# Kernel optimization log

Measured on AMD Instinct MI355X. Metric: run time of the kernel, lower is better.

The kernel has to match this reference:

```python
import jax, jax.numpy as jnp
import numpy as np

B, N, D, C = 1, 512, 128, 128
EPS = 1e-5


def _layernorm(x, g, b):
    m = jnp.mean(x, axis=-1, keepdims=True)
    v = jnp.mean(jnp.square(x - m), axis=-1, keepdims=True)
    return (x - m) * jax.lax.rsqrt(v + EPS) * g + b


def setup_inputs() -> dict:
    key = jax.random.key(0)
    ks = jax.random.split(key, 14)
    sD = 1.0 / np.sqrt(D)
    sC = 1.0 / np.sqrt(C)

    def w(k, shape, scale):
        return jax.random.normal(k, shape, dtype=jnp.float32) * scale

    return {
        "x": jax.random.normal(ks[0], (B, N, N, D), dtype=jnp.float32),
        "ln_in_g": jnp.ones((D,), jnp.float32),
        "ln_in_b": jnp.zeros((D,), jnp.float32),
        "ln_out_g": jnp.ones((C,), jnp.float32),
        "ln_out_b": jnp.zeros((C,), jnp.float32),
        "Wl": w(ks[1], (D, C), sD), "bl": w(ks[2], (C,), 0.02),
        "Wr": w(ks[3], (D, C), sD), "br": w(ks[4], (C,), 0.02),
        "Wo": w(ks[5], (C, D), sC), "bo": w(ks[6], (D,), 0.02),
        "Wlg": w(ks[7], (D, C), sD), "blg": w(ks[8], (C,), 0.02),
        "Wrg": w(ks[9], (D, C), sD), "brg": w(ks[10], (C,), 0.02),
        "Wog": w(ks[11], (D, D), sD), "bog": w(ks[12], (D,), 0.02),
    }


def reference(x, ln_in_g, ln_in_b, ln_out_g, ln_out_b,
              Wl, bl, Wr, br, Wo, bo, Wlg, blg, Wrg, brg, Wog, bog):
    # x: [B, N, N, D] pair representation
    xn = _layernorm(x, ln_in_g, ln_in_b)
    left = jax.nn.sigmoid(xn @ Wlg + blg) * (xn @ Wl + bl)    # [B,N,N,C]
    right = jax.nn.sigmoid(xn @ Wrg + brg) * (xn @ Wr + br)   # [B,N,N,C]
    # type='out': contract over k (rows): out[b,i,j,c] = sum_k left[b,k,i,c]*right[b,k,j,c]
    out = jnp.einsum('bkic,bkjc->bijc', left, right)           # [B,N,N,C]
    out = jax.nn.sigmoid(xn @ Wog + bog) * (_layernorm(out, ln_out_g, ln_out_b) @ Wo + bo)
    return out
```

## Files before the change

kernel.cpp:

```cpp
#include <hip/hip_runtime.h>
#include <hip/hip_bf16.h>
#include <cstdint>
#include <cstddef>

typedef unsigned short u16;
typedef short bf16x8 __attribute__((ext_vector_type(8)));
typedef float f32x4 __attribute__((ext_vector_type(4)));

constexpr int Ns = 512;
constexpr int Dd = 128;
constexpr int Cc = 128;
#define EPSV 1e-5f

__device__ __forceinline__ u16 f2bf(float f){
    __hip_bfloat16 h = __float2bfloat16(f);
    return *reinterpret_cast<u16*>(&h);
}
__device__ __forceinline__ float bf2f(u16 h){
    return __uint_as_float(((uint32_t)h) << 16);
}
__device__ __forceinline__ float sigmoidf_(float x){
    return __builtin_amdgcn_rcpf(1.0f + __expf(-x));
}

#define LDS_FENCE do {                                         \
    asm volatile("s_waitcnt lgkmcnt(0)" ::: "memory");         \
    __builtin_amdgcn_sched_barrier(0);                         \
} while (0)

__global__ void k_prep(const float* __restrict__ Wl, const float* __restrict__ Wlg,
                       const float* __restrict__ Wr, const float* __restrict__ Wrg,
                       const float* __restrict__ Wog, const float* __restrict__ Wo,
                       u16* __restrict__ Wt){
    int idx = blockIdx.x * 256 + threadIdx.x;
    if (idx >= 6 * 16384) return;
    int m = idx >> 14; int nk = idx & 16383; int n = nk >> 7; int k = nk & 127;
    const float* W = (m == 0) ? Wl : (m == 1) ? Wlg : (m == 2) ? Wr
                   : (m == 3) ? Wrg : (m == 4) ? Wog : Wo;
    Wt[idx] = f2bf(W[k * Cc + n]);
}

__global__ __launch_bounds__(256) void k1(
    const float* __restrict__ x, const float* __restrict__ g_ln, const float* __restrict__ b_ln,
    const u16* __restrict__ Wt,
    const float* __restrict__ bl, const float* __restrict__ blg,
    const float* __restrict__ br, const float* __restrict__ brg,
    const float* __restrict__ bog,
    u16* __restrict__ left, u16* __restrict__ right, u16* __restrict__ og)
{
    __shared__ u16  SB[8704];
    __shared__ float gln[128], bln[128];

    const int t   = threadIdx.x;
    const int bid = blockIdx.x;
    const int a0  = (bid >> 6) << 3;
    const int b0  = (bid & 63) << 3;
    const int w = t >> 6, l = t & 63;
    const int lrow = l & 15, g = l >> 4;
    const int nb = w * 32;
    const int orow = g << 2;
    const int kb = a0 >> 3;

    const int r = t >> 2, q = t & 3;
    const int aa = a0 + (r & 7), bb = b0 + (r >> 3);
    const float4* xrow = reinterpret_cast<const float4*>(x + ((size_t)aa * Ns + bb) * Dd);
    float4 xv[8];
#pragma unroll
    for (int i2 = 0; i2 < 8; ++i2) xv[i2] = xrow[q + 4 * i2];
    if (t < 128){ gln[t] = g_ln[t]; bln[t] = b_ln[t]; }

    float s1 = 0.f, s2 = 0.f;
#pragma unroll
    for (int i2 = 0; i2 < 8; ++i2){
        float4 v = xv[i2];
        s1 += v.x + v.y + v.z + v.w;
        s2 += v.x * v.x + v.y * v.y + v.z * v.z + v.w * v.w;
    }
    s1 += __shfl_xor(s1, 1); s1 += __shfl_xor(s1, 2);
    s2 += __shfl_xor(s2, 1); s2 += __shfl_xor(s2, 2);
    const float mm  = s1 * (1.0f / 128.0f);
    const float rsv = rsqrtf(s2 * (1.0f / 128.0f) - mm * mm + EPSV);
    __syncthreads();
#pragma unroll
    for (int i2 = 0; i2 < 8; ++i2){
        const int d = (q + 4 * i2) * 4;
        ushort4 o;
        o.x = f2bf((xv[i2].x - mm) * rsv * gln[d + 0] + bln[d + 0]);
        o.y = f2bf((xv[i2].y - mm) * rsv * gln[d + 1] + bln[d + 1]);
        o.z = f2bf((xv[i2].z - mm) * rsv * gln[d + 2] + bln[d + 2]);
        o.w = f2bf((xv[i2].w - mm) * rsv * gln[d + 3] + bln[d + 3]);
        *reinterpret_cast<ushort4*>(&SB[r * 136 + d]) = o;
    }
    __syncthreads();

    bf16x8 af[4][4];
#pragma unroll
    for (int ks = 0; ks < 4; ++ks)
#pragma unroll
        for (int rf = 0; rf < 4; ++rf)
            af[ks][rf] = *reinterpret_cast<const bf16x8*>(&SB[(rf * 16 + lrow) * 136 + ks * 32 + g * 8]);
    __syncthreads();

    u16* SBw = &SB[w * 32 * 68];
    const f32x4 zero4 = {0.f, 0.f, 0.f, 0.f};
    f32x4 aV[4], aG[4];

    auto GEMM1 = [&](const u16* WV, const u16* WG, int cf){
        const int col = nb + cf * 16 + lrow;
#pragma unroll
        for (int rf = 0; rf < 4; ++rf){ aV[rf] = zero4; aG[rf] = zero4; }
#pragma unroll
        for (int ks = 0; ks < 4; ++ks){
            bf16x8 bv = *reinterpret_cast<const bf16x8*>(WV + (size_t)col * 128 + ks * 32 + g * 8);
            bf16x8 bg = *reinterpret_cast<const bf16x8*>(WG + (size_t)col * 128 + ks * 32 + g * 8);
#pragma unroll
            for (int rf = 0; rf < 4; ++rf)
                aV[rf] = __builtin_amdgcn_mfma_f32_16x16x32_bf16(af[ks][rf], bv, aV[rf], 0, 0, 0);
#pragma unroll
            for (int rf = 0; rf < 4; ++rf)
                aG[rf] = __builtin_amdgcn_mfma_f32_16x16x32_bf16(af[ks][rf], bg, aG[rf], 0, 0, 0);
        }
    };
    auto STW = [&](const float* bV, const float* bG, int cf){
        const int cl2 = cf * 16 + lrow;
        const int col = nb + cl2;
        const float bVv = bV[col], bGv = bG[col];
#pragma unroll
        for (int rf = 0; rf < 4; ++rf){
            ushort4 pk;
#pragma unroll
            for (int j = 0; j < 4; ++j){
                const float vv = aV[rf][j] + bVv;
                const float gg = aG[rf][j] + bGv;
                ((u16*)&pk)[j] = f2bf(sigmoidf_(gg) * vv);
            }
            *reinterpret_cast<ushort4*>(&SBw[cl2 * 68 + rf * 16 + orow]) = pk;
        }
    };
    auto STORE = [&](u16* dst){
#pragma unroll
        for (int it = 0; it < 4; ++it){
            const int cl2 = it * 8 + (l >> 3);
            const int s   = l & 7;
            int4 v = *reinterpret_cast<const int4*>(&SBw[cl2 * 68 + s * 8]);
            *reinterpret_cast<int4*>(dst + (((size_t)(nb + cl2) * 64 + kb) * Ns + b0) * 8 + s * 8) = v;
        }
    };

    GEMM1(Wt,             Wt + 16384,     0); STW(bl, blg, 0);
    GEMM1(Wt,             Wt + 16384,     1); STW(bl, blg, 1);
    LDS_FENCE;
    STORE(left);
    LDS_FENCE;
    GEMM1(Wt + 2 * 16384, Wt + 3 * 16384, 0); STW(br, brg, 0);
    GEMM1(Wt + 2 * 16384, Wt + 3 * 16384, 1); STW(br, brg, 1);
    LDS_FENCE;
    STORE(right);
    __syncthreads();

    const u16* WO = Wt + (size_t)4 * 16384;
#pragma unroll 1
    for (int cf = 0; cf < 2; ++cf){
        const int col = nb + cf * 16 + lrow;
#pragma unroll
        for (int rf = 0; rf < 4; ++rf) aV[rf] = zero4;
#pragma unroll
        for (int ks = 0; ks < 4; ++ks){
            bf16x8 bv = *reinterpret_cast<const bf16x8*>(WO + (size_t)col * 128 + ks * 32 + g * 8);
#pragma unroll
            for (int rf = 0; rf < 4; ++rf)
                aV[rf] = __builtin_amdgcn_mfma_f32_16x16x32_bf16(af[ks][rf], bv, aV[rf], 0, 0, 0);
        }
        const float bOv = bog[col];
#pragma unroll
        for (int rf = 0; rf < 4; ++rf)
#pragma unroll
            for (int j = 0; j < 4; ++j){
                const int row = rf * 16 + orow + j;
                SB[row * 132 + col] = f2bf(sigmoidf_(aV[rf][j] + bOv));
            }
    }
    __syncthreads();
    const int bsub = t >> 5, c4 = (t & 31) * 4;
#pragma unroll
    for (int a = 0; a < 8; ++a){
        const int row = bsub * 8 + a;
        int2 v = *reinterpret_cast<const int2*>(&SB[row * 132 + c4]);
        *reinterpret_cast<int2*>(og + (((size_t)(a0 + a) * Ns) + (b0 + bsub)) * Cc + c4) = v;
    }
}

#define K2_LOAD(AF, BF, KS) do {                                                    \
    const size_t kbrow_ = (size_t)((KS) * 4 + lkb) * Ns;                            \
    _Pragma("unroll") for (int rf = 0; rf < 4; ++rf)                                \
        AF[rf] = *reinterpret_cast<const bf16x8*>(Lc + (kbrow_ + ib + rf * 16 + lrow) * 8); \
    _Pragma("unroll") for (int cf = 0; cf < 4; ++cf)                                \
        BF[cf] = *reinterpret_cast<const bf16x8*>(Rc + (kbrow_ + jb + cf * 16 + lrow) * 8); \
} while (0)

#define K2_MM(AF, BF) do {                                                          \
    _Pragma("unroll") for (int rf = 0; rf < 4; ++rf)                                \
    _Pragma("unroll") for (int cf = 0; cf < 4; ++cf)                                \
        acc[rf][cf] = __builtin_amdgcn_mfma_f32_16x16x32_bf16(AF[rf], BF[cf], acc[rf][cf], 0, 0, 0); \
} while (0)

__global__ __launch_bounds__(256) void k2(const u16* __restrict__ left,
                                          const u16* __restrict__ right,
                                          u16* __restrict__ om)
{
    __shared__ u16 sO[128][136];
    const int bid = blockIdx.x;
    const int xcd = bid & 7, idxx = bid >> 3;
    const int virt = xcd * 256 + idxx;
    const int c    = virt >> 4;
    const int tile = virt & 15;
    const int iy = tile >> 2, jx = tile & 3;
    const int t = threadIdx.x, w = t >> 6, l = t & 63;
    const int wr = w >> 1, wc = w & 1;
    const int ib = iy * 128 + wr * 64;
    const int jb = jx * 128 + wc * 64;
    const int lrow = l & 15, lkb = l >> 4;
    const u16* Lc = left  + (size_t)c * (Ns * Ns);
    const u16* Rc = right + (size_t)c * (Ns * Ns);
    const f32x4 zero4 = {0.f, 0.f, 0.f, 0.f};
    f32x4 acc[4][4];
#pragma unroll
    for (int rf = 0; rf < 4; ++rf)
#pragma unroll
        for (int cf = 0; cf < 4; ++cf) acc[rf][cf] = zero4;

    bf16x8 a0f[4], b0f[4], a1f[4], b1f[4];
    K2_LOAD(a0f, b0f, 0);
#pragma unroll
    for (int ks = 0; ks < 16; ks += 2){
        K2_LOAD(a1f, b1f, ks + 1);
        K2_MM(a0f, b0f);
        if (ks + 2 < 16) K2_LOAD(a0f, b0f, ks + 2);
        K2_MM(a1f, b1f);
    }

    const int orow = (l >> 4) << 2;
#pragma unroll
    for (int rf = 0; rf < 4; ++rf)
#pragma unroll
        for (int j2 = 0; j2 < 4; ++j2){
            const int rloc = wr * 64 + rf * 16 + orow + j2;
#pragma unroll
            for (int cf = 0; cf < 4; ++cf)
                sO[rloc][wc * 64 + cf * 16 + lrow] = f2bf(acc[rf][cf][j2]);
        }
    __syncthreads();
    u16* obase = om + (size_t)c * Ns * Ns + (size_t)(iy * 128) * Ns + jx * 128;
#pragma unroll
    for (int s = 0; s < 8; ++s){
        const int gg = s * 256 + t;
        const int row = gg >> 4, co = (gg & 15) * 8;
        int4 v = *reinterpret_cast<const int4*>(&sO[row][co]);
        *reinterpret_cast<int4*>(obase + (size_t)row * Ns + co) = v;
    }
}

__global__ __launch_bounds__(256) void k3(
    const u16* __restrict__ om, const u16* __restrict__ og, const u16* __restrict__ Wt,
    const float* __restrict__ g2, const float* __restrict__ b2, const float* __restrict__ bo,
    float* __restrict__ out)
{
    __shared__ char smem[34816];
    u16* X = reinterpret_cast<u16*>(smem);
    u16* O = reinterpret_cast<u16*>(smem) + 8704;
    __shared__ float sg2[128], sb2[128];
    const int i  = blockIdx.y;
    const int j0 = blockIdx.x * 64;
    const int t  = threadIdx.x;
    if (t < 128){ sg2[t] = g2[t]; sb2[t] = b2[t]; }
    {
        const int c = t >> 1, jh = (t & 1) * 32;
        const u16* src = om + (size_t)c * Ns * Ns + (size_t)i * Ns + j0 + jh;
#pragma unroll
        for (int s = 0; s < 8; ++s){
            ushort4 v = reinterpret_cast<const ushort4*>(src)[s];
            const int jj = jh + s * 4;
            X[(jj + 0) * 136 + c] = v.x; X[(jj + 1) * 136 + c] = v.y;
            X[(jj + 2) * 136 + c] = v.z; X[(jj + 3) * 136 + c] = v.w;
        }
    }
    {
        const int jj = t >> 2, qq = t & 3;
        const u16* src = og + ((size_t)i * Ns + j0 + jj) * Cc + qq * 32;
#pragma unroll
        for (int s = 0; s < 4; ++s)
            *reinterpret_cast<int4*>(&O[jj * 136 + qq * 32 + s * 8]) = reinterpret_cast<const int4*>(src)[s];
    }
    __syncthreads();
    const int r = t >> 2, q = t & 3;
    {
        float s1 = 0.f, s2v = 0.f;
#pragma unroll
        for (int e = 0; e < 32; ++e){
            const float v = bf2f(X[r * 136 + q * 32 + e]);
            s1 += v; s2v += v * v;
        }
        s1  += __shfl_xor(s1, 1);  s1  += __shfl_xor(s1, 2);
        s2v += __shfl_xor(s2v, 1); s2v += __shfl_xor(s2v, 2);
        const float mm  = s1 * (1.0f / 128.0f);
        const float rsv = rsqrtf(s2v * (1.0f / 128.0f) - mm * mm + EPSV);
#pragma unroll
        for (int e = 0; e < 32; ++e){
            const int cc = q * 32 + e;
            const float v = bf2f(X[r * 136 + cc]);
            X[r * 136 + cc] = f2bf((v - mm) * rsv * sg2[cc] + sb2[cc]);
        }
    }
    __syncthreads();
    const int w = t >> 6, l = t & 63;
    const int lrow = l & 15, lk = (l >> 4) << 3, nbv = w * 32, orow = (l >> 4) << 2;
    const u16* WO = Wt + (size_t)5 * 16384;
    const f32x4 zero4 = {0.f, 0.f, 0.f, 0.f};
    f32x4 acc[4][2];
#pragma unroll
    for (int rf = 0; rf < 4; ++rf)
#pragma unroll
        for (int cf = 0; cf < 2; ++cf) acc[rf][cf] = zero4;
#pragma unroll
    for (int ks = 0; ks < 4; ++ks){
        const int k0 = ks * 32 + lk;
        bf16x8 af[4];
#pragma unroll
        for (int rf = 0; rf < 4; ++rf)
            af[rf] = *reinterpret_cast<const bf16x8*>(&X[(rf * 16 + lrow) * 136 + k0]);
#pragma unroll
        for (int cf = 0; cf < 2; ++cf){
            bf16x8 bv = *reinterpret_cast<const bf16x8*>(WO + (size_t)(nbv + cf * 16 + lrow) * 128 + k0);
#pragma unroll
            for (int rf = 0; rf < 4; ++rf)
                acc[rf][cf] = __builtin_amdgcn_mfma_f32_16x16x32_bf16(af[rf], bv, acc[rf][cf], 0, 0, 0);
        }
    }
    float gv[2][4][4];
#pragma unroll
    for (int cf = 0; cf < 2; ++cf){
        const int cg = nbv + cf * 16 + lrow;
        const float bov = bo[cg];
#pragma unroll
        for (int rf = 0; rf < 4; ++rf)
#pragma unroll
            for (int j = 0; j < 4; ++j){
                const int row = rf * 16 + orow + j;
                gv[cf][rf][j] = bf2f(O[row * 136 + cg]) * (acc[rf][cf][j] + bov);
            }
    }
    __syncthreads();
    float* sF = reinterpret_cast<float*>(smem);
#pragma unroll
    for (int cf = 0; cf < 2; ++cf){
        const int cg = nbv + cf * 16 + lrow;
#pragma unroll
        for (int rf = 0; rf < 4; ++rf)
#pragma unroll
            for (int j = 0; j < 4; ++j){
                const int row = rf * 16 + orow + j;
                sF[row * 128 + cg] = gv[cf][rf][j];
            }
    }
    __syncthreads();
    const float4* sF4 = reinterpret_cast<const float4*>(smem);
    float* obase = out + ((size_t)i * Ns + j0) * Cc;
#pragma unroll
    for (int s = 0; s < 8; ++s){
        const int gg = s * 256 + t;
        const int row = gg >> 5, co = (gg & 31) * 4;
        float4 v = sF4[gg];
        *reinterpret_cast<float4*>(obase + (size_t)row * Cc + co) = v;
    }
}

extern "C" void kernel_launch(void* const* d_in, const int* in_sizes, int n_in,
                              void* d_out, int out_size, void* d_ws, size_t ws_size,
                              hipStream_t stream)
{
    const float* x    = (const float*)d_in[0];
    const float* ling = (const float*)d_in[1];
    const float* linb = (const float*)d_in[2];
    const float* loutg= (const float*)d_in[3];
    const float* loutb= (const float*)d_in[4];
    const float* Wl   = (const float*)d_in[5];
    const float* bl   = (const float*)d_in[6];
    const float* Wr   = (const float*)d_in[7];
    const float* br   = (const float*)d_in[8];
    const float* Wo   = (const float*)d_in[9];
    const float* bo   = (const float*)d_in[10];
    const float* Wlg  = (const float*)d_in[11];
    const float* blg  = (const float*)d_in[12];
    const float* Wrg  = (const float*)d_in[13];
    const float* brg  = (const float*)d_in[14];
    const float* Wog  = (const float*)d_in[15];
    const float* bog  = (const float*)d_in[16];

    char* ws = (char*)d_ws;
    u16* Wt = (u16*)ws;
    const size_t off = 256 * 1024;
    const size_t SZ  = (size_t)33554432 * 2;
    u16* left  = (u16*)(ws + off);
    u16* right = (u16*)(ws + off + SZ);
    u16* og    = (u16*)(ws + off + 2 * SZ);
    u16* om    = (u16*)(ws + off + 3 * SZ);

    hipLaunchKernelGGL(k_prep, dim3(384), dim3(256), 0, stream, Wl, Wlg, Wr, Wrg, Wog, Wo, Wt);
    hipLaunchKernelGGL(k1, dim3(4096), dim3(256), 0, stream,
                       x, ling, linb, Wt, bl, blg, br, brg, bog, left, right, og);
    hipLaunchKernelGGL(k2, dim3(2048), dim3(256), 0, stream, left, right, om);
    hipLaunchKernelGGL(k3, dim3(8, 512), dim3(256), 0, stream, om, og, Wt, loutg, loutb, bo, (float*)d_out);
}
```

Measured before the change: 254.1 us.

## Double k1 tile to 16x8 pair rows with 512-thread blocks

The k1 block grows from 256 to 512 threads and now handles 16 a-rows by 8 b-columns, with two half-groups of four waves sharing the same weight columns. This halves the grid, so each block fetches the weight fragments once for twice as many rows. The left/right and og store paths are re-indexed so each block writes two kb blocks per column and uses wider int4 stores. In exchange, LDS per block doubles and each write to left/right is split into two shorter contiguous segments, which could hurt coalescing and occupancy.

```diff
diff --git a/kernel.cpp b/kernel.cpp
--- a/kernel.cpp
+++ b/kernel.cpp
@@ -40,7 +40,7 @@
     Wt[idx] = f2bf(W[k * Cc + n]);
 }
 
-__global__ __launch_bounds__(256) void k1(
+__global__ __launch_bounds__(512) void k1(
     const float* __restrict__ x, const float* __restrict__ g_ln, const float* __restrict__ b_ln,
     const u16* __restrict__ Wt,
     const float* __restrict__ bl, const float* __restrict__ blg,
@@ -48,21 +48,22 @@
     const float* __restrict__ bog,
     u16* __restrict__ left, u16* __restrict__ right, u16* __restrict__ og)
 {
-    __shared__ u16  SB[8704];
+    __shared__ u16  SB[17408];
     __shared__ float gln[128], bln[128];
 
     const int t   = threadIdx.x;
     const int bid = blockIdx.x;
-    const int a0  = (bid >> 6) << 3;
+    const int a0  = (bid >> 6) << 4;
     const int b0  = (bid & 63) << 3;
     const int w = t >> 6, l = t & 63;
     const int lrow = l & 15, g = l >> 4;
-    const int nb = w * 32;
+    const int h  = w >> 2;
+    const int nb = (w & 3) * 32;
     const int orow = g << 2;
-    const int kb = a0 >> 3;
+    const int kb2 = a0 >> 3;
 
     const int r = t >> 2, q = t & 3;
-    const int aa = a0 + (r & 7), bb = b0 + (r >> 3);
+    const int aa = a0 + (r & 15), bb = b0 + (r >> 4);
     const float4* xrow = reinterpret_cast<const float4*>(x + ((size_t)aa * Ns + bb) * Dd);
     float4 xv[8];
 #pragma unroll
@@ -98,7 +99,8 @@
     for (int ks = 0; ks < 4; ++ks)
 #pragma unroll
         for (int rf = 0; rf < 4; ++rf)
-            af[ks][rf] = *reinterpret_cast<const bf16x8*>(&SB[(rf * 16 + lrow) * 136 + ks * 32 + g * 8]);
+            af[ks][rf] = *reinterpret_cast<const bf16x8*>(
+                &SB[(h * 64 + rf * 16 + lrow) * 136 + ks * 32 + g * 8]);
     __syncthreads();
 
     u16* SBw = &SB[w * 32 * 68];
@@ -140,10 +142,14 @@
     auto STORE = [&](u16* dst){
 #pragma unroll
         for (int it = 0; it < 4; ++it){
-            const int cl2 = it * 8 + (l >> 3);
-            const int s   = l & 7;
-            int4 v = *reinterpret_cast<const int4*>(&SBw[cl2 * 68 + s * 8]);
-            *reinterpret_cast<int4*>(dst + (((size_t)(nb + cl2) * 64 + kb) * Ns + b0) * 8 + s * 8) = v;
+            const int idx   = it * 64 + l;
+            const int col_l = idx >> 3;
+            const int kbi   = (idx >> 2) & 1;
+            const int b_rel = idx & 3;
+            int4 v = *reinterpret_cast<const int4*>(&SBw[col_l * 68 + b_rel * 16 + kbi * 8]);
+            const size_t base = (((size_t)(nb + col_l) * 64 + kb2 + kbi) * Ns
+                                 + b0 + h * 4 + b_rel) * 8;
+            *reinterpret_cast<int4*>(dst + base) = v;
         }
     };
 
@@ -176,17 +182,19 @@
         for (int rf = 0; rf < 4; ++rf)
 #pragma unroll
             for (int j = 0; j < 4; ++j){
-                const int row = rf * 16 + orow + j;
-                SB[row * 132 + col] = f2bf(sigmoidf_(aV[rf][j] + bOv));
+                const int lr = h * 64 + rf * 16 + orow + j;
+                SB[lr * 132 + col] = f2bf(sigmoidf_(aV[rf][j] + bOv));
             }
     }
     __syncthreads();
-    const int bsub = t >> 5, c4 = (t & 31) * 4;
-#pragma unroll
-    for (int a = 0; a < 8; ++a){
-        const int row = bsub * 8 + a;
-        int2 v = *reinterpret_cast<const int2*>(&SB[row * 132 + c4]);
-        *reinterpret_cast<int2*>(og + (((size_t)(a0 + a) * Ns) + (b0 + bsub)) * Cc + c4) = v;
+    {
+        const int lr = t >> 2, c4 = (t & 3) * 32;
+        const size_t gb = ((size_t)(a0 + (lr & 15)) * Ns + b0 + (lr >> 4)) * Cc + c4;
+#pragma unroll
+        for (int s = 0; s < 4; ++s){
+            int4 v = *reinterpret_cast<const int4*>(&SB[lr * 132 + c4 + s * 8]);
+            *reinterpret_cast<int4*>(og + gb + s * 8) = v;
+        }
     }
 }
 
@@ -406,7 +414,7 @@
     u16* om    = (u16*)(ws + off + 3 * SZ);
 
     hipLaunchKernelGGL(k_prep, dim3(384), dim3(256), 0, stream, Wl, Wlg, Wr, Wrg, Wog, Wo, Wt);
-    hipLaunchKernelGGL(k1, dim3(4096), dim3(256), 0, stream,
+    hipLaunchKernelGGL(k1, dim3(2048), dim3(512), 0, stream,
                        x, ling, linb, Wt, bl, blg, br, brg, bog, left, right, og);
     hipLaunchKernelGGL(k2, dim3(2048), dim3(256), 0, stream, left, right, om);
     hipLaunchKernelGGL(k3, dim3(8, 512), dim3(256), 0, stream, om, og, Wt, loutg, loutb, bo, (float*)d_out);
```

Result: slower. 288.2 us (+13.4%).

## Recompute output gate in final kernel instead of storing gate tensor

Applied to the files above, without the earlier changes.

The output-gate GEMM (xn @ Wog) and its sigmoid move out of the first kernel. The final kernel now rereads x, recomputes the input layernorm, and runs the gate GEMM next to the Wo projection. This removes the bf16 gate intermediate (64 MB written and read back) and the extra shared-memory transpose in k1. In exchange k3 reads fp32 x (128 MB), does the layernorm and GEMM a second time, and uses more registers for the doubled accumulators.

```diff
diff --git a/kernel.cpp b/kernel.cpp
--- a/kernel.cpp
+++ b/kernel.cpp
@@ -45,8 +45,7 @@
     const u16* __restrict__ Wt,
     const float* __restrict__ bl, const float* __restrict__ blg,
     const float* __restrict__ br, const float* __restrict__ brg,
-    const float* __restrict__ bog,
-    u16* __restrict__ left, u16* __restrict__ right, u16* __restrict__ og)
+    u16* __restrict__ left, u16* __restrict__ right)
 {
     __shared__ u16  SB[8704];
     __shared__ float gln[128], bln[128];
@@ -156,38 +155,6 @@
     GEMM1(Wt + 2 * 16384, Wt + 3 * 16384, 1); STW(br, brg, 1);
     LDS_FENCE;
     STORE(right);
-    __syncthreads();
-
-    const u16* WO = Wt + (size_t)4 * 16384;
-#pragma unroll 1
-    for (int cf = 0; cf < 2; ++cf){
-        const int col = nb + cf * 16 + lrow;
-#pragma unroll
-        for (int rf = 0; rf < 4; ++rf) aV[rf] = zero4;
-#pragma unroll
-        for (int ks = 0; ks < 4; ++ks){
-            bf16x8 bv = *reinterpret_cast<const bf16x8*>(WO + (size_t)col * 128 + ks * 32 + g * 8);
-#pragma unroll
-            for (int rf = 0; rf < 4; ++rf)
-                aV[rf] = __builtin_amdgcn_mfma_f32_16x16x32_bf16(af[ks][rf], bv, aV[rf], 0, 0, 0);
-        }
-        const float bOv = bog[col];
-#pragma unroll
-        for (int rf = 0; rf < 4; ++rf)
-#pragma unroll
-            for (int j = 0; j < 4; ++j){
-                const int row = rf * 16 + orow + j;
-                SB[row * 132 + col] = f2bf(sigmoidf_(aV[rf][j] + bOv));
-            }
-    }
-    __syncthreads();
-    const int bsub = t >> 5, c4 = (t & 31) * 4;
-#pragma unroll
-    for (int a = 0; a < 8; ++a){
-        const int row = bsub * 8 + a;
-        int2 v = *reinterpret_cast<const int2*>(&SB[row * 132 + c4]);
-        *reinterpret_cast<int2*>(og + (((size_t)(a0 + a) * Ns) + (b0 + bsub)) * Cc + c4) = v;
-    }
 }
 
 #define K2_LOAD(AF, BF, KS) do {                                                    \
@@ -261,18 +228,39 @@
 }
 
 __global__ __launch_bounds__(256) void k3(
-    const u16* __restrict__ om, const u16* __restrict__ og, const u16* __restrict__ Wt,
-    const float* __restrict__ g2, const float* __restrict__ b2, const float* __restrict__ bo,
+    const u16* __restrict__ om, const float* __restrict__ x,
+    const float* __restrict__ g1, const float* __restrict__ b1,
+    const u16* __restrict__ Wt,
+    const float* __restrict__ g2, const float* __restrict__ b2,
+    const float* __restrict__ bogv, const float* __restrict__ bo,
     float* __restrict__ out)
 {
     __shared__ char smem[34816];
-    u16* X = reinterpret_cast<u16*>(smem);
-    u16* O = reinterpret_cast<u16*>(smem) + 8704;
-    __shared__ float sg2[128], sb2[128];
+    u16* X  = reinterpret_cast<u16*>(smem);
+    u16* Xn = reinterpret_cast<u16*>(smem) + 8704;
+    __shared__ float sg2[128], sb2[128], sg1[128], sb1[128];
     const int i  = blockIdx.y;
     const int j0 = blockIdx.x * 64;
     const int t  = threadIdx.x;
-    if (t < 128){ sg2[t] = g2[t]; sb2[t] = b2[t]; }
+    if (t < 128){ sg2[t] = g2[t]; sb2[t] = b2[t]; sg1[t] = g1[t]; sb1[t] = b1[t]; }
+
+    const int r = t >> 2, q = t & 3;
+    const float4* xr = reinterpret_cast<const float4*>(x + ((size_t)i * Ns + j0 + r) * Dd);
+    float4 xv[8];
+#pragma unroll
+    for (int i2 = 0; i2 < 8; ++i2) xv[i2] = xr[q + 4 * i2];
+    float s1 = 0.f, s2 = 0.f;
+#pragma unroll
+    for (int i2 = 0; i2 < 8; ++i2){
+        float4 v = xv[i2];
+        s1 += v.x + v.y + v.z + v.w;
+        s2 += v.x * v.x + v.y * v.y + v.z * v.z + v.w * v.w;
+    }
+    s1 += __shfl_xor(s1, 1); s1 += __shfl_xor(s1, 2);
+    s2 += __shfl_xor(s2, 1); s2 += __shfl_xor(s2, 2);
+    const float mm1  = s1 * (1.0f / 128.0f);
+    const float rsv1 = rsqrtf(s2 * (1.0f / 128.0f) - mm1 * mm1 + EPSV);
+
     {
         const int c = t >> 1, jh = (t & 1) * 32;
         const u16* src = om + (size_t)c * Ns * Ns + (size_t)i * Ns + j0 + jh;
@@ -284,26 +272,29 @@
             X[(jj + 2) * 136 + c] = v.z; X[(jj + 3) * 136 + c] = v.w;
         }
     }
+    __syncthreads();
+#pragma unroll
+    for (int i2 = 0; i2 < 8; ++i2){
+        const int d = (q + 4 * i2) * 4;
+        ushort4 o;
+        o.x = f2bf((xv[i2].x - mm1) * rsv1 * sg1[d + 0] + sb1[d + 0]);
+        o.y = f2bf((xv[i2].y - mm1) * rsv1 * sg1[d + 1] + sb1[d + 1]);
+        o.z = f2bf((xv[i2].z - mm1) * rsv1 * sg1[d + 2] + sb1[d + 2]);
+        o.w = f2bf((xv[i2].w - mm1) * rsv1 * sg1[d + 3] + sb1[d + 3]);
+        *reinterpret_cast<ushort4*>(&Xn[r * 136 + d]) = o;
+    }
+    __syncthreads();
     {
-        const int jj = t >> 2, qq = t & 3;
-        const u16* src = og + ((size_t)i * Ns + j0 + jj) * Cc + qq * 32;
-#pragma unroll
-        for (int s = 0; s < 4; ++s)
-            *reinterpret_cast<int4*>(&O[jj * 136 + qq * 32 + s * 8]) = reinterpret_cast<const int4*>(src)[s];
-    }
-    __syncthreads();
-    const int r = t >> 2, q = t & 3;
-    {
-        float s1 = 0.f, s2v = 0.f;
+        float a1 = 0.f, a2 = 0.f;
 #pragma unroll
         for (int e = 0; e < 32; ++e){
             const float v = bf2f(X[r * 136 + q * 32 + e]);
-            s1 += v; s2v += v * v;
-        }
-        s1  += __shfl_xor(s1, 1);  s1  += __shfl_xor(s1, 2);
-        s2v += __shfl_xor(s2v, 1); s2v += __shfl_xor(s2v, 2);
-        const float mm  = s1 * (1.0f / 128.0f);
-        const float rsv = rsqrtf(s2v * (1.0f / 128.0f) - mm * mm + EPSV);
+            a1 += v; a2 += v * v;
+        }
+        a1 += __shfl_xor(a1, 1); a1 += __shfl_xor(a1, 2);
+        a2 += __shfl_xor(a2, 1); a2 += __shfl_xor(a2, 2);
+        const float mm  = a1 * (1.0f / 128.0f);
+        const float rsv = rsqrtf(a2 * (1.0f / 128.0f) - mm * mm + EPSV);
 #pragma unroll
         for (int e = 0; e < 32; ++e){
             const int cc = q * 32 + e;
@@ -312,42 +303,49 @@
         }
     }
     __syncthreads();
+
     const int w = t >> 6, l = t & 63;
     const int lrow = l & 15, lk = (l >> 4) << 3, nbv = w * 32, orow = (l >> 4) << 2;
-    const u16* WO = Wt + (size_t)5 * 16384;
+    const u16* WOG = Wt + (size_t)4 * 16384;
+    const u16* WO  = Wt + (size_t)5 * 16384;
     const f32x4 zero4 = {0.f, 0.f, 0.f, 0.f};
-    f32x4 acc[4][2];
+    f32x4 accW[4][2], accO[4][2];
 #pragma unroll
     for (int rf = 0; rf < 4; ++rf)
 #pragma unroll
-        for (int cf = 0; cf < 2; ++cf) acc[rf][cf] = zero4;
+        for (int cf = 0; cf < 2; ++cf){ accW[rf][cf] = zero4; accO[rf][cf] = zero4; }
 #pragma unroll
     for (int ks = 0; ks < 4; ++ks){
         const int k0 = ks * 32 + lk;
-        bf16x8 af[4];
-#pragma unroll
-        for (int rf = 0; rf < 4; ++rf)
-            af[rf] = *reinterpret_cast<const bf16x8*>(&X[(rf * 16 + lrow) * 136 + k0]);
+        bf16x8 af[4], afn[4];
+#pragma unroll
+        for (int rf = 0; rf < 4; ++rf){
+            af[rf]  = *reinterpret_cast<const bf16x8*>(&X[(rf * 16 + lrow) * 136 + k0]);
+            afn[rf] = *reinterpret_cast<const bf16x8*>(&Xn[(rf * 16 + lrow) * 136 + k0]);
+        }
 #pragma unroll
         for (int cf = 0; cf < 2; ++cf){
-            bf16x8 bv = *reinterpret_cast<const bf16x8*>(WO + (size_t)(nbv + cf * 16 + lrow) * 128 + k0);
+            const int colg = nbv + cf * 16 + lrow;
+            bf16x8 bv = *reinterpret_cast<const bf16x8*>(WO  + (size_t)colg * 128 + k0);
+            bf16x8 bg = *reinterpret_cast<const bf16x8*>(WOG + (size_t)colg * 128 + k0);
 #pragma unroll
             for (int rf = 0; rf < 4; ++rf)
-                acc[rf][cf] = __builtin_amdgcn_mfma_f32_16x16x32_bf16(af[rf], bv, acc[rf][cf], 0, 0, 0);
+                accW[rf][cf] = __builtin_amdgcn_mfma_f32_16x16x32_bf16(af[rf], bv, accW[rf][cf], 0, 0, 0);
+#pragma unroll
+            for (int rf = 0; rf < 4; ++rf)
+                accO[rf][cf] = __builtin_amdgcn_mfma_f32_16x16x32_bf16(afn[rf], bg, accO[rf][cf], 0, 0, 0);
         }
     }
     float gv[2][4][4];
 #pragma unroll
     for (int cf = 0; cf < 2; ++cf){
         const int cg = nbv + cf * 16 + lrow;
-        const float bov = bo[cg];
+        const float bov = bo[cg], bogc = bogv[cg];
 #pragma unroll
         for (int rf = 0; rf < 4; ++rf)
 #pragma unroll
-            for (int j = 0; j < 4; ++j){
-                const int row = rf * 16 + orow + j;
-                gv[cf][rf][j] = bf2f(O[row * 136 + cg]) * (acc[rf][cf][j] + bov);
-            }
+            for (int j = 0; j < 4; ++j)
+                gv[cf][rf][j] = sigmoidf_(accO[rf][cf][j] + bogc) * (accW[rf][cf][j] + bov);
     }
     __syncthreads();
     float* sF = reinterpret_cast<float*>(smem);
@@ -402,12 +400,12 @@
     const size_t SZ  = (size_t)33554432 * 2;
     u16* left  = (u16*)(ws + off);
     u16* right = (u16*)(ws + off + SZ);
-    u16* og    = (u16*)(ws + off + 2 * SZ);
-    u16* om    = (u16*)(ws + off + 3 * SZ);
+    u16* om    = (u16*)(ws + off + 2 * SZ);
 
     hipLaunchKernelGGL(k_prep, dim3(384), dim3(256), 0, stream, Wl, Wlg, Wr, Wrg, Wog, Wo, Wt);
     hipLaunchKernelGGL(k1, dim3(4096), dim3(256), 0, stream,
-                       x, ling, linb, Wt, bl, blg, br, brg, bog, left, right, og);
+                       x, ling, linb, Wt, bl, blg, br, brg, left, right);
     hipLaunchKernelGGL(k2, dim3(2048), dim3(256), 0, stream, left, right, om);
-    hipLaunchKernelGGL(k3, dim3(8, 512), dim3(256), 0, stream, om, og, Wt, loutg, loutb, bo, (float*)d_out);
-}
+    hipLaunchKernelGGL(k3, dim3(8, 512), dim3(256), 0, stream,
+                       om, x, ling, linb, Wt, loutg, loutb, bog, bo, (float*)d_out);
+}
```

Result: slower. 266.7 us (+5.0%).
